# Performance work log

Measured on AMD Instinct MI355X. Metric: run time of the kernel, lower is better.

## Reference

```python
import jax, jax.numpy as jnp
import numpy as np


def setup_inputs() -> dict:
    key = jax.random.key(0)
    k1, k2, k3, k4 = jax.random.split(key, 4)
    n_smps, n_fcns, d_in, d_out = 16384, 2048, 32, 32
    GAIN = 1e-5  # xavier gain used by init_wts / init_offsets
    x = jax.random.normal(k1, (n_smps, d_in), dtype=jnp.float32)
    ctrs = jax.random.normal(k2, (n_fcns, d_in), dtype=jnp.float32)
    wts = jax.random.normal(k3, (n_fcns, d_in, d_out), dtype=jnp.float32) * GAIN
    offsets = jax.random.normal(k4, (n_fcns, d_out), dtype=jnp.float32) * GAIN
    return {"x": x, "ctrs": ctrs, "wts": wts, "offsets": offsets, "k": 4}


def reference(x, ctrs, wts, offsets, k):
    # --- knn_do equivalent (done under no_grad in torch) ---
    # squared Euclidean distance: (n_smps, n_fcns)
    x_sg = jax.lax.stop_gradient(x)
    c_sg = jax.lax.stop_gradient(ctrs)
    d2 = (jnp.sum(x_sg * x_sg, axis=1, keepdims=True)
          - 2.0 * (x_sg @ c_sg.T)
          + jnp.sum(c_sg * c_sg, axis=1)[None, :])
    _, idx = jax.lax.top_k(-d2, k)  # (n_smps, k), nearest centers

    # --- gather per-neighbor local linear models ---
    sel_wts = wts[idx]        # (n_smps, k, d_in, d_out)
    sel_ctrs = ctrs[idx]      # (n_smps, k, d_in)
    sel_offs = offsets[idx]   # (n_smps, k, d_out)

    applied_wts = jnp.sum(sel_wts, axis=1)  # (n_smps, d_in, d_out)
    # offsets minus sum over neighbors/d_in of wts * ctrs
    applied_offsets = (jnp.sum(sel_offs, axis=1)
                       - jnp.einsum('nkde,nkd->ne', sel_wts, sel_ctrs))
    # y = x @ applied_wts + applied_offsets, per sample
    y = jnp.einsum('nde,nd->ne', applied_wts, x) + applied_offsets
    return y
```

## Files before the change

kernel.cpp:

```cpp
#include <hip/hip_runtime.h>
#include <math.h>

typedef short bf16x8 __attribute__((ext_vector_type(8)));
typedef float f32x4  __attribute__((ext_vector_type(4)));

#define N_SMPS 16384
#define N_FCNS 2048
#define D_IN 32
#define D_OUT 32
#define KNN 4
#define SPLITS 4
#define CPS 512
#define TILES 32
#define POOL 48

__device__ __forceinline__ unsigned umin_u(unsigned a, unsigned b) { return a < b ? a : b; }
__device__ __forceinline__ unsigned umax_u(unsigned a, unsigned b) { return a > b ? a : b; }

__device__ __forceinline__ unsigned short bf16_rne(float f) {
  unsigned b = __float_as_uint(f);
  unsigned r = b + 0x7FFFu + ((b >> 16) & 1u);
  return (unsigned short)(r >> 16);
}

#define OFF_XH   0u
#define OFF_CH   1048576u
#define OFF_HB   (OFF_CH + 131072u)
#define OFF_WB   (OFF_HB + 8192u)
#define OFF_POOL (OFF_WB + 4194304u)

#define NX4 (N_SMPS * D_IN / 4)
#define NC4 (N_FCNS * D_IN / 4)
#define NW4 (N_FCNS * D_IN * D_OUT / 4)
#define NTOT (NX4 + NC4 + NW4)

__global__ __launch_bounds__(256) void k_prep(
    const float* __restrict__ x, const float* __restrict__ ctrs,
    const float* __restrict__ wts,
    unsigned short* __restrict__ xh, unsigned short* __restrict__ ch,
    unsigned short* __restrict__ wb, float* __restrict__ hb)
{
  const int gt = blockIdx.x * 256 + threadIdx.x;
  const float* src; unsigned short* dst; int i4;
  if (gt < NX4)            { src = x;    dst = xh; i4 = gt; }
  else if (gt < NX4 + NC4) { src = ctrs; dst = ch; i4 = gt - NX4; }
  else                     { src = wts;  dst = wb; i4 = gt - (NX4 + NC4); }
  float4 v = ((const float4*)src)[i4];
  ushort4 o;
  o.x = bf16_rne(v.x); o.y = bf16_rne(v.y);
  o.z = bf16_rne(v.z); o.w = bf16_rne(v.w);
  ((ushort4*)dst)[i4] = o;

  if (gt < N_FCNS) {
    const float4* cp4 = (const float4*)(ctrs + (size_t)gt * D_IN);
    float a = 0.f;
    #pragma unroll
    for (int q = 0; q < 8; ++q) {
      float4 c = cp4[q];
      a += c.x * c.x + c.y * c.y + c.z * c.z + c.w * c.w;
    }
    hb[gt] = -0.5f * a;
  }
}

__global__ __launch_bounds__(256) void k_topk(
    const unsigned short* __restrict__ xh, const unsigned short* __restrict__ ch,
    const float* __restrict__ hb, unsigned* __restrict__ pool)
{
  __shared__ unsigned s_cand[SPLITS][16][16][4];

  const int tid = threadIdx.x;
  const int lane = tid & 63;
  const int w = __builtin_amdgcn_readfirstlane(tid >> 6);
  const int col = lane & 15;
  const int quad = lane >> 4;
  const int sbase = blockIdx.x * 16;
  const int nbase0 = w * CPS;

  const bf16x8 ah =
      *(const bf16x8*)(xh + (size_t)(sbase + col) * D_IN + quad * 8);

  unsigned ls[4][4];
  #pragma unroll
  for (int r = 0; r < 4; ++r)
    #pragma unroll
    for (int e = 0; e < 4; ++e) ls[r][e] = 0u;

  #pragma unroll 2
  for (int t = 0; t < TILES; ++t) {
    const int nb = nbase0 + t * 16;
    const bf16x8 bh =
        *(const bf16x8*)(ch + (size_t)(nb + col) * D_IN + quad * 8);
    const float hbv = hb[nb + col];
    f32x4 acc = {0.f, 0.f, 0.f, 0.f};
    acc = __builtin_amdgcn_mfma_f32_16x16x32_bf16(ah, bh, acc, 0, 0, 0);
    const unsigned tc = (unsigned)(t * 16 + col);
    #pragma unroll
    for (int r = 0; r < 4; ++r) {
      const float u = acc[r] + hbv;
      unsigned b = __float_as_uint(u);
      unsigned m = b ^ ((unsigned)((int)b >> 31) | 0x80000000u);
      unsigned key = (m & 0xFFFFFE00u) | tc;
      unsigned t0 = umin_u(ls[r][0], key); ls[r][0] = umax_u(ls[r][0], key);
      unsigned t1 = umin_u(ls[r][1], t0);  ls[r][1] = umax_u(ls[r][1], t0);
      unsigned t2 = umin_u(ls[r][2], t1);  ls[r][2] = umax_u(ls[r][2], t1);
      ls[r][3] = umax_u(ls[r][3], t2);
    }
  }

  #pragma unroll
  for (int r = 0; r < 4; ++r) {
    const int row = quad * 4 + r;
    *(uint4*)&s_cand[w][row][col][0] =
        make_uint4(ls[r][0], ls[r][1], ls[r][2], ls[r][3]);
  }
  __syncthreads();

  if (tid < 128) {
    const int sl = tid >> 3;
    const int g  = tid & 7;
    const int wv = g >> 1;
    const int chh = (g & 1) * 8;
    unsigned q0 = 0, q1 = 0, q2 = 0, q3 = 0, q4 = 0, q5 = 0;
    #pragma unroll
    for (int c2 = 0; c2 < 8; ++c2) {
      uint4 kv = *(const uint4*)&s_cand[wv][sl][chh + c2][0];
      unsigned ks[4] = {kv.x, kv.y, kv.z, kv.w};
      #pragma unroll
      for (int e = 0; e < 4; ++e) {
        unsigned key = ks[e];
        unsigned t0 = umin_u(q0, key); q0 = umax_u(q0, key);
        unsigned t1 = umin_u(q1, t0);  q1 = umax_u(q1, t0);
        unsigned t2 = umin_u(q2, t1);  q2 = umax_u(q2, t1);
        unsigned t3 = umin_u(q3, t2);  q3 = umax_u(q3, t2);
        unsigned t4 = umin_u(q4, t3);  q4 = umax_u(q4, t3);
        q5 = umax_u(q5, t4);
      }
    }
    unsigned* op = pool + (size_t)(sbase + sl) * POOL + g * 6;
    op[0] = q0; op[1] = q1; op[2] = q2;
    op[3] = q3; op[4] = q4; op[5] = q5;
  }
}

#define K2_BLOCK 256
#define K2_SAMPLES 8

__global__ __launch_bounds__(K2_BLOCK) void k_apply(
    const float* __restrict__ x, const float* __restrict__ ctrs,
    const unsigned short* __restrict__ wb, const float* __restrict__ offs,
    const unsigned* __restrict__ pool, float* __restrict__ y)
{
  __shared__ double s_pd2[K2_SAMPLES][POOL];
  __shared__ int    s_pix[K2_SAMPLES][POOL];
  __shared__ int    s_sel[K2_SAMPLES][KNN];
  __shared__ float  s_diff[K2_SAMPLES][KNN][D_IN + 1];
  __shared__ float4 s_part[K2_SAMPLES][KNN][D_OUT / 4];

  const int tid = threadIdx.x;
  const int sbase = blockIdx.x * K2_SAMPLES;

  for (int c = tid; c < K2_SAMPLES * POOL; c += K2_BLOCK) {
    const int sl = c / POOL;
    const int p = c - sl * POOL;
    const unsigned key = pool[(size_t)(sbase + sl) * POOL + p];
    const int wv = p / 12;
    const int j = wv * CPS + (int)(key & 0x1FFu);
    const float4* xp4 = (const float4*)(x + (size_t)(sbase + sl) * D_IN);
    const float4* cp4 = (const float4*)(ctrs + (size_t)j * D_IN);
    double d2a = 0.0, d2b = 0.0;
    #pragma unroll
    for (int q = 0; q < 8; ++q) {
      float4 cv = cp4[q];
      float4 xv = xp4[q];
      double df0 = (double)xv.x - (double)cv.x;
      double df1 = (double)xv.y - (double)cv.y;
      double df2 = (double)xv.z - (double)cv.z;
      double df3 = (double)xv.w - (double)cv.w;
      d2a = fma(df0, df0, d2a);
      d2b = fma(df1, df1, d2b);
      d2a = fma(df2, df2, d2a);
      d2b = fma(df3, df3, d2b);
    }
    s_pd2[sl][p] = d2a + d2b;
    s_pix[sl][p] = j;
  }
  __syncthreads();

  if (tid < K2_SAMPLES) {
    double bd[4]; int b4[4];
    #pragma unroll
    for (int e = 0; e < 4; ++e) { bd[e] = 1e300; b4[e] = 0x7fffffff; }
    for (int m = 0; m < POOL; ++m) {
      const double d2 = s_pd2[tid][m];
      const int j = s_pix[tid][m];
      bool ins = (d2 < bd[3]) || (d2 == bd[3] && j < b4[3]);
      if (ins) {
        bd[3] = d2; b4[3] = j;
        #pragma unroll
        for (int q = 3; q > 0; --q) {
          bool sw = (bd[q] < bd[q - 1]) ||
                    (bd[q] == bd[q - 1] && b4[q] < b4[q - 1]);
          if (sw) {
            double td = bd[q]; bd[q] = bd[q - 1]; bd[q - 1] = td;
            int    tj = b4[q]; b4[q] = b4[q - 1]; b4[q - 1] = tj;
          }
        }
      }
    }
    #pragma unroll
    for (int q = 0; q < 4; ++q) s_sel[tid][q] = b4[q];
  }
  __syncthreads();

  #pragma unroll
  for (int r = 0; r < K2_SAMPLES * KNN * D_IN / K2_BLOCK; ++r) {
    int v = r * K2_BLOCK + tid;
    int d = v & 31; int p = v >> 5;
    int sl = p >> 2; int j = p & 3;
    int f = s_sel[sl][j];
    s_diff[sl][j][d] =
        x[(size_t)(sbase + sl) * D_IN + d] - ctrs[(size_t)f * D_IN + d];
  }
  __syncthreads();

  const int sl = tid >> 5;
  const int j  = (tid >> 3) & 3;
  const int eq = tid & 7;
  const int s = sbase + sl;

  const int f = s_sel[sl][j];
  const uint2* wp = (const uint2*)(wb + (size_t)f * (D_IN * D_OUT));
  float4 acc = ((const float4*)(offs + (size_t)f * D_OUT))[eq];
  #pragma unroll
  for (int d = 0; d < D_IN; ++d) {
    uint2 wv = wp[d * 8 + eq];
    float w0 = __uint_as_float(wv.x << 16);
    float w1 = __uint_as_float(wv.x & 0xFFFF0000u);
    float w2 = __uint_as_float(wv.y << 16);
    float w3 = __uint_as_float(wv.y & 0xFFFF0000u);
    float xc = s_diff[sl][j][d];
    acc.x = fmaf(xc, w0, acc.x);
    acc.y = fmaf(xc, w1, acc.y);
    acc.z = fmaf(xc, w2, acc.z);
    acc.w = fmaf(xc, w3, acc.w);
  }
  s_part[sl][j][eq] = acc;
  __syncthreads();

  if (j == 0) {
    float4 a = s_part[sl][0][eq], b = s_part[sl][1][eq];
    float4 c = s_part[sl][2][eq], e = s_part[sl][3][eq];
    float4 o;
    o.x = (a.x + b.x) + (c.x + e.x);
    o.y = (a.y + b.y) + (c.y + e.y);
    o.z = (a.z + b.z) + (c.z + e.z);
    o.w = (a.w + b.w) + (c.w + e.w);
    ((float4*)(y + (size_t)s * D_OUT))[eq] = o;
  }
}

extern "C" void kernel_launch(void* const* d_in, const int* in_sizes, int n_in,
                              void* d_out, int out_size, void* d_ws, size_t ws_size,
                              hipStream_t stream) {
  const float* x    = (const float*)d_in[0];
  const float* ctrs = (const float*)d_in[1];
  const float* wts  = (const float*)d_in[2];
  const float* offs = (const float*)d_in[3];
  float* y = (float*)d_out;

  char* ws = (char*)d_ws;
  unsigned short* xh = (unsigned short*)(ws + OFF_XH);
  unsigned short* ch = (unsigned short*)(ws + OFF_CH);
  float*          hb = (float*)(ws + OFF_HB);
  unsigned short* wb = (unsigned short*)(ws + OFF_WB);
  unsigned*     pool = (unsigned*)(ws + OFF_POOL);

  k_prep<<<NTOT / 256, 256, 0, stream>>>(x, ctrs, wts, xh, ch, wb, hb);
  k_topk<<<N_SMPS / 16, 256, 0, stream>>>(xh, ch, hb, pool);
  k_apply<<<N_SMPS / K2_SAMPLES, K2_BLOCK, 0, stream>>>(x, ctrs, wb, offs,
                                                        pool, y);
}
```

Measured before the change: 116.4 us.

## Fuse bf16 prep into top-k kernel and remap blocks to split-per-block

Removes the separate prep kernel: x and centers are converted to bf16 on the fly inside the top-k loop, center norms are computed per block into shared memory, and the wts bf16 conversion is spread across top-k blocks. The grid is remapped so each block covers 64 samples against one center split, with each wave doing its own 16-sample merge. This saves one launch and the intermediate bf16 round trip, but adds redundant fp32 center loads and conversions in every block.

Measured after the change: 136.9 us. 17.6% more time.

```diff
diff --git a/kernel.cpp b/kernel.cpp
--- a/kernel.cpp
+++ b/kernel.cpp
@@ -23,62 +23,68 @@
   return (unsigned short)(r >> 16);
 }
 
-#define OFF_XH   0u
-#define OFF_CH   1048576u
-#define OFF_HB   (OFF_CH + 131072u)
-#define OFF_WB   (OFF_HB + 8192u)
-#define OFF_POOL (OFF_WB + 4194304u)
-
-#define NX4 (N_SMPS * D_IN / 4)
-#define NC4 (N_FCNS * D_IN / 4)
+#define OFF_WB   0u
+#define OFF_POOL 4194304u
+
 #define NW4 (N_FCNS * D_IN * D_OUT / 4)
-#define NTOT (NX4 + NC4 + NW4)
-
-__global__ __launch_bounds__(256) void k_prep(
+
+__global__ __launch_bounds__(256) void k_topk(
     const float* __restrict__ x, const float* __restrict__ ctrs,
-    const float* __restrict__ wts,
-    unsigned short* __restrict__ xh, unsigned short* __restrict__ ch,
-    unsigned short* __restrict__ wb, float* __restrict__ hb)
+    const float* __restrict__ wts, unsigned short* __restrict__ wb,
+    unsigned* __restrict__ pool)
 {
-  const int gt = blockIdx.x * 256 + threadIdx.x;
-  const float* src; unsigned short* dst; int i4;
-  if (gt < NX4)            { src = x;    dst = xh; i4 = gt; }
-  else if (gt < NX4 + NC4) { src = ctrs; dst = ch; i4 = gt - NX4; }
-  else                     { src = wts;  dst = wb; i4 = gt - (NX4 + NC4); }
-  float4 v = ((const float4*)src)[i4];
-  ushort4 o;
-  o.x = bf16_rne(v.x); o.y = bf16_rne(v.y);
-  o.z = bf16_rne(v.z); o.w = bf16_rne(v.w);
-  ((ushort4*)dst)[i4] = o;
-
-  if (gt < N_FCNS) {
-    const float4* cp4 = (const float4*)(ctrs + (size_t)gt * D_IN);
-    float a = 0.f;
-    #pragma unroll
-    for (int q = 0; q < 8; ++q) {
-      float4 c = cp4[q];
-      a += c.x * c.x + c.y * c.y + c.z * c.z + c.w * c.w;
-    }
-    hb[gt] = -0.5f * a;
-  }
-}
-
-__global__ __launch_bounds__(256) void k_topk(
-    const unsigned short* __restrict__ xh, const unsigned short* __restrict__ ch,
-    const float* __restrict__ hb, unsigned* __restrict__ pool)
-{
-  __shared__ unsigned s_cand[SPLITS][16][16][4];
+  __shared__ float    s_hb[CPS];
+  __shared__ unsigned s_cand[4][16][16][4];
 
   const int tid = threadIdx.x;
   const int lane = tid & 63;
   const int w = __builtin_amdgcn_readfirstlane(tid >> 6);
   const int col = lane & 15;
   const int quad = lane >> 4;
-  const int sbase = blockIdx.x * 16;
-  const int nbase0 = w * CPS;
-
-  const bf16x8 ah =
-      *(const bf16x8*)(xh + (size_t)(sbase + col) * D_IN + quad * 8);
+  const int sp = blockIdx.x & 3;
+  const int sg = blockIdx.x >> 2;
+  const int sbase = sg * 64 + w * 16;
+  const int nbase0 = sp * CPS;
+
+  {
+    const float4* wsrc = (const float4*)wts;
+    ushort4* wdst = (ushort4*)wb;
+    #pragma unroll
+    for (int r = 0; r < 2; ++r) {
+      const int i4 = blockIdx.x * 512 + r * 256 + tid;
+      float4 v = wsrc[i4];
+      ushort4 o;
+      o.x = bf16_rne(v.x); o.y = bf16_rne(v.y);
+      o.z = bf16_rne(v.z); o.w = bf16_rne(v.w);
+      wdst[i4] = o;
+    }
+  }
+
+  #pragma unroll
+  for (int r = 0; r < 2; ++r) {
+    const int rl = r * 256 + tid;
+    if (rl < CPS) {
+      const float4* cp4 = (const float4*)(ctrs + (size_t)(nbase0 + rl) * D_IN);
+      float a = 0.f;
+      #pragma unroll
+      for (int q = 0; q < 8; ++q) {
+        float4 c = cp4[q];
+        a += c.x * c.x + c.y * c.y + c.z * c.z + c.w * c.w;
+      }
+      s_hb[rl] = -0.5f * a;
+    }
+  }
+
+  bf16x8 ah;
+  {
+    const float4* xp =
+        (const float4*)(x + (size_t)(sbase + col) * D_IN + quad * 8);
+    float4 v0 = xp[0], v1 = xp[1];
+    float xf[8] = {v0.x, v0.y, v0.z, v0.w, v1.x, v1.y, v1.z, v1.w};
+    #pragma unroll
+    for (int i = 0; i < 8; ++i) ah[i] = (short)bf16_rne(xf[i]);
+  }
+  __syncthreads();
 
   unsigned ls[4][4];
   #pragma unroll
@@ -88,13 +94,20 @@
 
   #pragma unroll 2
   for (int t = 0; t < TILES; ++t) {
-    const int nb = nbase0 + t * 16;
-    const bf16x8 bh =
-        *(const bf16x8*)(ch + (size_t)(nb + col) * D_IN + quad * 8);
-    const float hbv = hb[nb + col];
+    const int rl = t * 16 + col;
+    const float4* cp =
+        (const float4*)(ctrs + (size_t)(nbase0 + rl) * D_IN + quad * 8);
+    float4 c0 = cp[0], c1 = cp[1];
+    float cf[8] = {c0.x, c0.y, c0.z, c0.w, c1.x, c1.y, c1.z, c1.w};
+    bf16x8 bh;
+    #pragma unroll
+    for (int i = 0; i < 8; ++i) bh[i] = (short)bf16_rne(cf[i]);
+    const float hbv = s_hb[rl];
+
     f32x4 acc = {0.f, 0.f, 0.f, 0.f};
     acc = __builtin_amdgcn_mfma_f32_16x16x32_bf16(ah, bh, acc, 0, 0, 0);
-    const unsigned tc = (unsigned)(t * 16 + col);
+
+    const unsigned tc = (unsigned)rl;
     #pragma unroll
     for (int r = 0; r < 4; ++r) {
       const float u = acc[r] + hbv;
@@ -116,15 +129,14 @@
   }
   __syncthreads();
 
-  if (tid < 128) {
-    const int sl = tid >> 3;
-    const int g  = tid & 7;
-    const int wv = g >> 1;
-    const int chh = (g & 1) * 8;
+  if (lane < 32) {
+    const int sl = lane >> 1;
+    const int half = lane & 1;
+    const int chh = half * 8;
     unsigned q0 = 0, q1 = 0, q2 = 0, q3 = 0, q4 = 0, q5 = 0;
     #pragma unroll
     for (int c2 = 0; c2 < 8; ++c2) {
-      uint4 kv = *(const uint4*)&s_cand[wv][sl][chh + c2][0];
+      uint4 kv = *(const uint4*)&s_cand[w][sl][chh + c2][0];
       unsigned ks[4] = {kv.x, kv.y, kv.z, kv.w};
       #pragma unroll
       for (int e = 0; e < 4; ++e) {
@@ -137,7 +149,7 @@
         q5 = umax_u(q5, t4);
       }
     }
-    unsigned* op = pool + (size_t)(sbase + sl) * POOL + g * 6;
+    unsigned* op = pool + (size_t)(sbase + sl) * POOL + (sp * 2 + half) * 6;
     op[0] = q0; op[1] = q1; op[2] = q2;
     op[3] = q3; op[4] = q4; op[5] = q5;
   }
@@ -270,14 +282,10 @@
   float* y = (float*)d_out;
 
   char* ws = (char*)d_ws;
-  unsigned short* xh = (unsigned short*)(ws + OFF_XH);
-  unsigned short* ch = (unsigned short*)(ws + OFF_CH);
-  float*          hb = (float*)(ws + OFF_HB);
   unsigned short* wb = (unsigned short*)(ws + OFF_WB);
   unsigned*     pool = (unsigned*)(ws + OFF_POOL);
 
-  k_prep<<<NTOT / 256, 256, 0, stream>>>(x, ctrs, wts, xh, ch, wb, hb);
-  k_topk<<<N_SMPS / 16, 256, 0, stream>>>(xh, ch, hb, pool);
+  k_topk<<<(N_SMPS / 64) * SPLITS, 256, 0, stream>>>(x, ctrs, wts, wb, pool);
   k_apply<<<N_SMPS / K2_SAMPLES, K2_BLOCK, 0, stream>>>(x, ctrs, wb, offs,
                                                         pool, y);
 }
```
